# Kernel optimization log

Measured on AMD Instinct MI355X. Metric: run time of the kernel, lower is better.

## Reference

```python
import jax, jax.numpy as jnp
import numpy as np

BATCH, SEQ_L, H, N = 16, 2048, 512, 64
DT_MIN, DT_MAX = 1e-3, 1e-1


def setup_inputs() -> dict:
    key = jax.random.key(0)
    ks = jax.random.split(key, 6)
    u = jax.random.normal(ks[0], (BATCH, SEQ_L, H), dtype=jnp.float32)
    # S4D diagonal init: stable real part, linearly spaced imaginary frequencies
    Lambda_real = -0.5 * jnp.ones((N,), dtype=jnp.float32)
    Lambda_imag = jnp.pi * jnp.arange(N, dtype=jnp.float32)
    B_real = jax.random.normal(ks[1], (H, N), dtype=jnp.float32) * (N ** -0.5)
    B_imag = jnp.zeros((H, N), dtype=jnp.float32)
    C_real = jax.random.normal(ks[2], (H, N), dtype=jnp.float32) * 0.5
    C_imag = jax.random.normal(ks[3], (H, N), dtype=jnp.float32) * 0.5
    log_dt = (jax.random.uniform(ks[4], (H,), dtype=jnp.float32)
              * (np.float32(np.log(DT_MAX)) - np.float32(np.log(DT_MIN)))
              + np.float32(np.log(DT_MIN)))
    D = jax.random.normal(ks[5], (H,), dtype=jnp.float32) * 0.01
    return {"u": u, "Lambda_real": Lambda_real, "Lambda_imag": Lambda_imag,
            "B_real": B_real, "B_imag": B_imag, "C_real": C_real,
            "C_imag": C_imag, "log_dt": log_dt, "D": D}


def reference(u, Lambda_real, Lambda_imag, B_real, B_imag, C_real, C_imag, log_dt, D):
    # u: (B, L, H)
    Lseq = u.shape[1]
    Lam = Lambda_real + 1j * Lambda_imag            # (N,)
    Bc = B_real + 1j * B_imag                        # (H, N)
    Cc = C_real + 1j * C_imag                        # (H, N)
    dt = jnp.exp(log_dt)                             # (H,)

    # ZOH discretization (matches step(): Ab = exp(dt*Lam), Bb = B*(Ab-1)/(Lam+eps))
    dtA = dt[:, None] * Lam[None, :]                 # (H, N)
    Ab = jnp.exp(dtA)
    Bb = Bc * (Ab - 1.0) / (Lam[None, :] + 1e-8)

    # Vandermonde over all channels at once: V[h,n,l] = exp(dt_h * Lam_n * l)
    ell = jnp.arange(Lseq, dtype=jnp.float32)
    V = jnp.exp(dtA[:, :, None] * ell[None, None, :])  # (H, N, L) complex
    K = jnp.einsum('hn,hnl->hl', Cc * Bb, V).real       # (H, L) real kernel

    # Causal FFT convolution along time
    x = jnp.swapaxes(u, -1, -2)                      # (B, H, L)
    nfft = 2 * Lseq
    Xf = jnp.fft.rfft(x, n=nfft)                     # (B, H, nfft/2+1)
    Kf = jnp.fft.rfft(K, n=nfft)                     # (H, nfft/2+1)
    y = jnp.fft.irfft(Xf * Kf[None], n=nfft)[..., :Lseq]

    y = y + x * D[None, :, None]                     # skip connection
    return jnp.swapaxes(y, -1, -2)                   # (B, L, H)
```

## Files before the change

### kernel.cpp

```cpp
#include <hip/hip_runtime.h>
#include <hip/hip_bf16.h>


#define BSZ 16
#define LSEQ 2048
#define HCH 512
#define NST 64
#define NF 4096

__device__ __forceinline__ int WD(int i) { return 2 * i + ((i >> 4) << 1); }

__device__ __forceinline__ float2 cadd(float2 a, float2 b) { return make_float2(a.x + b.x, a.y + b.y); }
__device__ __forceinline__ float2 csub(float2 a, float2 b) { return make_float2(a.x - b.x, a.y - b.y); }
__device__ __forceinline__ float2 cmul(float2 a, float c, float s) {
    return make_float2(a.x * c - a.y * s, a.x * s + a.y * c);
}
__device__ __forceinline__ float2 cmul2(float2 a, float2 b) {
    return make_float2(a.x * b.x - a.y * b.y, a.x * b.y + a.y * b.x);
}

__device__ __forceinline__ void sincos_red(float a, float* s, float* c) {
    double ad = (double)a;
    double q = rint(ad * 0.15915494309189535);
    float r = (float)(ad - q * 6.283185307179586);
    __sincosf(r, s, c);
}

template <bool INV>
__device__ __forceinline__ void dft8_tail(float2 t0, float2 t1, float2 t2, float2 t3,
                                          float2 t4, float2 t5, float2 t6, float2 t7,
                                          float2& A0, float2& A1, float2& A2, float2& A3,
                                          float2& A4, float2& A5, float2& A6, float2& A7)
{
    const float S = 0.70710678118654752f;
    float2 u0 = cadd(t0, t2), u2 = csub(t0, t2);
    float2 u1 = cadd(t1, t3), u3 = csub(t1, t3);
    A0 = cadd(u0, u1); A4 = csub(u0, u1);
    if constexpr (!INV) {
        A2 = make_float2(u2.x + u3.y, u2.y - u3.x);
        A6 = make_float2(u2.x - u3.y, u2.y + u3.x);
    } else {
        A2 = make_float2(u2.x - u3.y, u2.y + u3.x);
        A6 = make_float2(u2.x + u3.y, u2.y - u3.x);
    }
    float2 b0 = t4, b1, b2, b3;
    if constexpr (!INV) {
        b1 = make_float2(S * (t5.x + t5.y), S * (t5.y - t5.x));
        b2 = make_float2(t6.y, -t6.x);
        b3 = make_float2(S * (t7.y - t7.x), -S * (t7.x + t7.y));
    } else {
        b1 = make_float2(S * (t5.x - t5.y), S * (t5.y + t5.x));
        b2 = make_float2(-t6.y, t6.x);
        b3 = make_float2(-S * (t7.x + t7.y), S * (t7.x - t7.y));
    }
    float2 v0 = cadd(b0, b2), v2 = csub(b0, b2);
    float2 v1 = cadd(b1, b3), v3 = csub(b1, b3);
    A1 = cadd(v0, v1); A5 = csub(v0, v1);
    if constexpr (!INV) {
        A3 = make_float2(v2.x + v3.y, v2.y - v3.x);
        A7 = make_float2(v2.x - v3.y, v2.y + v3.x);
    } else {
        A3 = make_float2(v2.x - v3.y, v2.y + v3.x);
        A7 = make_float2(v2.x + v3.y, v2.y - v3.x);
    }
}

template <int SIDX, bool INV, bool HALF, int NT>
__device__ __forceinline__ void fft8_stage(float* z, int t)
{
    constexpr int lgQ = 9 - 3 * SIDX;
    constexpr int Q = 1 << lgQ;
    constexpr int ITERS = 512 / NT;
    const float asc = -1.5339807878856412e-3f * (float)(1 << (3 * SIDX));
#pragma unroll
    for (int it = 0; it < ITERS; ++it) {
        const int bb = t + NT * it;
        const int j = bb & (Q - 1);
        const int base = ((bb >> lgQ) << (lgQ + 3)) + j;
        float s1, c1;
        __sincosf(asc * (float)j, &s1, &c1);
        if constexpr (INV) s1 = -s1;
        const float c2 = c1 * c1 - s1 * s1, s2 = 2.f * c1 * s1;
        const float c3 = c1 * c2 - s1 * s2, s3 = c1 * s2 + s1 * c2;
        const float c4 = c2 * c2 - s2 * s2, s4 = 2.f * c2 * s2;
        const float c5 = c2 * c3 - s2 * s3, s5 = c2 * s3 + s2 * c3;
        const float c6 = c3 * c3 - s3 * s3, s6 = 2.f * c3 * s3;
        const float c7 = c3 * c4 - s3 * s4, s7 = c3 * s4 + s3 * c4;
        float2 a0 = *(float2*)&z[WD(base + 0 * Q)];
        float2 a1 = *(float2*)&z[WD(base + 1 * Q)];
        float2 a2 = *(float2*)&z[WD(base + 2 * Q)];
        float2 a3 = *(float2*)&z[WD(base + 3 * Q)];
        float2 a4, a5, a6, a7;
        if constexpr (!(HALF && !INV)) {
            a4 = *(float2*)&z[WD(base + 4 * Q)];
            a5 = *(float2*)&z[WD(base + 5 * Q)];
            a6 = *(float2*)&z[WD(base + 6 * Q)];
            a7 = *(float2*)&z[WD(base + 7 * Q)];
        }
        if constexpr (INV) {
            a1 = cmul(a1, c1, s1); a2 = cmul(a2, c2, s2); a3 = cmul(a3, c3, s3);
            a4 = cmul(a4, c4, s4); a5 = cmul(a5, c5, s5); a6 = cmul(a6, c6, s6);
            a7 = cmul(a7, c7, s7);
        }
        float2 t0, t1, t2, t3, t4, t5, t6, t7;
        if constexpr (HALF && !INV) {
            t0 = a0; t4 = a0; t1 = a1; t5 = a1; t2 = a2; t6 = a2; t3 = a3; t7 = a3;
        } else {
            t0 = cadd(a0, a4); t4 = csub(a0, a4);
            t1 = cadd(a1, a5); t5 = csub(a1, a5);
            t2 = cadd(a2, a6); t6 = csub(a2, a6);
            t3 = cadd(a3, a7); t7 = csub(a3, a7);
        }
        float2 A0, A1, A2, A3, A4, A5, A6, A7;
        dft8_tail<INV>(t0, t1, t2, t3, t4, t5, t6, t7, A0, A1, A2, A3, A4, A5, A6, A7);
        if constexpr (!INV) {
            A1 = cmul(A1, c1, s1); A2 = cmul(A2, c2, s2); A3 = cmul(A3, c3, s3);
            A4 = cmul(A4, c4, s4); A5 = cmul(A5, c5, s5); A6 = cmul(A6, c6, s6);
            A7 = cmul(A7, c7, s7);
        }
        *(float2*)&z[WD(base + 0 * Q)] = A0;
        *(float2*)&z[WD(base + 1 * Q)] = A1;
        *(float2*)&z[WD(base + 2 * Q)] = A2;
        *(float2*)&z[WD(base + 3 * Q)] = A3;
        if constexpr (!(HALF && INV)) {
            *(float2*)&z[WD(base + 4 * Q)] = A4;
            *(float2*)&z[WD(base + 5 * Q)] = A5;
            *(float2*)&z[WD(base + 6 * Q)] = A6;
            *(float2*)&z[WD(base + 7 * Q)] = A7;
        }
    }
}

template <int NT>
__device__ __forceinline__ void mid_stage(float* z, const float2* __restrict__ kf, int t)
{
    constexpr int ITERS = 512 / NT;
#pragma unroll
    for (int it = 0; it < ITERS; ++it) {
        const int bb = t + NT * it;
        const int base = bb * 8;
        float2 a[8];
#pragma unroll
        for (int r = 0; r < 8; ++r) a[r] = *(float2*)&z[WD(base + r)];
        float2 t0 = cadd(a[0], a[4]), t4 = csub(a[0], a[4]);
        float2 t1 = cadd(a[1], a[5]), t5 = csub(a[1], a[5]);
        float2 t2 = cadd(a[2], a[6]), t6 = csub(a[2], a[6]);
        float2 t3 = cadd(a[3], a[7]), t7 = csub(a[3], a[7]);
        float2 A0, A1, A2, A3, A4, A5, A6, A7;
        dft8_tail<false>(t0, t1, t2, t3, t4, t5, t6, t7, A0, A1, A2, A3, A4, A5, A6, A7);
        const float2* kp = kf + base;
        A0 = cmul2(A0, kp[0]); A1 = cmul2(A1, kp[1]);
        A2 = cmul2(A2, kp[2]); A3 = cmul2(A3, kp[3]);
        A4 = cmul2(A4, kp[4]); A5 = cmul2(A5, kp[5]);
        A6 = cmul2(A6, kp[6]); A7 = cmul2(A7, kp[7]);
        t0 = cadd(A0, A4); t4 = csub(A0, A4);
        t1 = cadd(A1, A5); t5 = csub(A1, A5);
        t2 = cadd(A2, A6); t6 = csub(A2, A6);
        t3 = cadd(A3, A7); t7 = csub(A3, A7);
        float2 X0, X1, X2, X3, X4, X5, X6, X7;
        dft8_tail<true>(t0, t1, t2, t3, t4, t5, t6, t7, X0, X1, X2, X3, X4, X5, X6, X7);
        *(float2*)&z[WD(base + 0)] = X0;
        *(float2*)&z[WD(base + 1)] = X1;
        *(float2*)&z[WD(base + 2)] = X2;
        *(float2*)&z[WD(base + 3)] = X3;
        *(float2*)&z[WD(base + 4)] = X4;
        *(float2*)&z[WD(base + 5)] = X5;
        *(float2*)&z[WD(base + 6)] = X6;
        *(float2*)&z[WD(base + 7)] = X7;
    }
}

__global__ __launch_bounds__(512) void k_front(const float* __restrict__ lam_r,
                                               const float* __restrict__ lam_i,
                                               const float* __restrict__ Br,
                                               const float* __restrict__ Bi,
                                               const float* __restrict__ Cr,
                                               const float* __restrict__ Ci,
                                               const float* __restrict__ log_dt,
                                               float* __restrict__ gKf,
                                               const float* __restrict__ u,
                                               float* __restrict__ gut)
{
    const int bid = blockIdx.x;
    const int t = threadIdx.x;
    __shared__ float lds[8704];
    __shared__ float sWr[NST], sWi[NST], sAr[NST], sAi[NST], sDr[NST], sDi[NST];

    if (bid < HCH) {
        const int h = bid;
        if (t < NST) {
            const int n = t;
            float lr = lam_r[n], li = lam_i[n];
            float dt = __expf(log_dt[h]);
            float dar = dt * lr;
            float dai = dt * li;
            float e = __expf(dar);
            float sn, cs; sincos_red(dai, &sn, &cs);
            float Ar = e * cs, Ai = e * sn;
            float nr = Ar - 1.0f, ni = Ai;
            float br = Br[h * NST + n], bi = Bi[h * NST + n];
            float tr = br * nr - bi * ni;
            float ti = br * ni + bi * nr;
            float dr = lr + 1e-8f, di = li;
            float den = dr * dr + di * di;
            float bbr = (tr * dr + ti * di) / den;
            float bbi = (ti * dr - tr * di) / den;
            float cr = Cr[h * NST + n], ci = Ci[h * NST + n];
            sWr[n] = cr * bbr - ci * bbi;
            sWi[n] = cr * bbi + ci * bbr;
            sAr[n] = Ar; sAi[n] = Ai;
            sDr[n] = dar; sDi[n] = dai;
        }
        __syncthreads();

        const int l0 = 4 * t;
        float acc[4] = {0.f, 0.f, 0.f, 0.f};
        const float fl0 = (float)l0;
        for (int n = 0; n < NST; ++n) {
            float dar = sDr[n], dai = sDi[n];
            float ang = dai * fl0;
            float sn, cs; sincos_red(ang, &sn, &cs);
            float e = __expf(dar * fl0);
            float pr = e * cs, pi = e * sn;
            float Ar = sAr[n], Ai = sAi[n];
            float wr = sWr[n], wi = sWi[n];
#pragma unroll
            for (int k = 0; k < 4; ++k) {
                acc[k] += wr * pr - wi * pi;
                float npr = pr * Ar - pi * Ai;
                pi = pr * Ai + pi * Ar;
                pr = npr;
            }
        }
        *(float2*)&lds[WD(l0 + 0)] = make_float2(acc[0], 0.f);
        *(float2*)&lds[WD(l0 + 1)] = make_float2(acc[1], 0.f);
        *(float2*)&lds[WD(l0 + 2)] = make_float2(acc[2], 0.f);
        *(float2*)&lds[WD(l0 + 3)] = make_float2(acc[3], 0.f);
        __syncthreads();

        fft8_stage<0, false, true , 512>(lds, t); __syncthreads();
        fft8_stage<1, false, false, 512>(lds, t); __syncthreads();
        fft8_stage<2, false, false, 512>(lds, t); __syncthreads();
        fft8_stage<3, false, false, 512>(lds, t); __syncthreads();

        float2* outp = (float2*)gKf + (size_t)h * NF;
#pragma unroll
        for (int i = 0; i < 8; ++i) {
            int idx = t + 512 * i;
            outp[idx] = *(float2*)&lds[WD(idx)];
        }
    } else {
        float (*tile)[65] = (float (*)[65])lds;
        const int tid2 = bid - HCH;
        const int b  = tid2 >> 8;
        const int ht = ((tid2 >> 5) & 7) * 64;
        const int lt = (tid2 & 31) * 64;
        const int tx = t & 15;
        const int ty = t >> 4;
        const float* inb = u + (size_t)b * LSEQ * HCH;
        float* outb = gut + (size_t)b * HCH * LSEQ;
#pragma unroll
        for (int i = 0; i < 2; ++i) {
            int r = ty + 32 * i;
            float4 v = *(const float4*)&inb[(size_t)(lt + r) * HCH + ht + 4 * tx];
            tile[r][4 * tx + 0] = v.x;
            tile[r][4 * tx + 1] = v.y;
            tile[r][4 * tx + 2] = v.z;
            tile[r][4 * tx + 3] = v.w;
        }
        __syncthreads();
#pragma unroll
        for (int i = 0; i < 2; ++i) {
            int rp = ty + 32 * i;
            float4 o = make_float4(tile[4 * tx + 0][rp], tile[4 * tx + 1][rp],
                                   tile[4 * tx + 2][rp], tile[4 * tx + 3][rp]);
            *(float4*)&outb[(size_t)(ht + rp) * LSEQ + lt + 4 * tx] = o;
        }
    }
}

__global__ __launch_bounds__(256) void k_transpose_bwd(const float* __restrict__ in,
                                                       float* __restrict__ out)
{
    __shared__ float tile[64][65];
    const int b  = blockIdx.z;
    const int lt = blockIdx.x * 64;
    const int ht = blockIdx.y * 64;
    const int tx = threadIdx.x;
    const int ty = threadIdx.y;
    const float* inb = in + (size_t)b * HCH * LSEQ;
    float* outb = out + (size_t)b * LSEQ * HCH;
#pragma unroll
    for (int i = 0; i < 4; ++i) {
        int r = ty + 16 * i;
        float4 v = *(const float4*)&inb[(size_t)(ht + r) * LSEQ + lt + 4 * tx];
        tile[r][4 * tx + 0] = v.x;
        tile[r][4 * tx + 1] = v.y;
        tile[r][4 * tx + 2] = v.z;
        tile[r][4 * tx + 3] = v.w;
    }
    __syncthreads();
#pragma unroll
    for (int i = 0; i < 4; ++i) {
        int rp = ty + 16 * i;
        float4 o = make_float4(tile[4 * tx + 0][rp], tile[4 * tx + 1][rp],
                               tile[4 * tx + 2][rp], tile[4 * tx + 3][rp]);
        *(float4*)&outb[(size_t)(lt + rp) * HCH + ht + 4 * tx] = o;
    }
}

__global__ __launch_bounds__(512, 4) void k_fftconv(float* __restrict__ gut,
                                                    const float* __restrict__ gKf,
                                                    const float* __restrict__ gD)
{
    const int bid = blockIdx.x;
    const int b = bid >> 9;
    const int h = bid & (HCH - 1);
    const int t = threadIdx.x;
    __shared__ float z[8704];

    float* row0 = gut + ((size_t)(b * HCH) + h) * LSEQ;
    float* row1 = gut + ((size_t)((b + 8) * HCH) + h) * LSEQ;

    float4 u0k = ((const float4*)row0)[t];
    float4 u1k = ((const float4*)row1)[t];
    {
        int l = 4 * t;
        *(float2*)&z[WD(l + 0)] = make_float2(u0k.x, u1k.x);
        *(float2*)&z[WD(l + 1)] = make_float2(u0k.y, u1k.y);
        *(float2*)&z[WD(l + 2)] = make_float2(u0k.z, u1k.z);
        *(float2*)&z[WD(l + 3)] = make_float2(u0k.w, u1k.w);
    }
    __syncthreads();

    fft8_stage<0, false, true , 512>(z, t); __syncthreads();
    fft8_stage<1, false, false, 512>(z, t); __syncthreads();
    fft8_stage<2, false, false, 512>(z, t); __syncthreads();
    mid_stage<512>(z, (const float2*)gKf + (size_t)h * NF, t); __syncthreads();
    fft8_stage<2, true, false, 512>(z, t); __syncthreads();
    fft8_stage<1, true, false, 512>(z, t); __syncthreads();
    fft8_stage<0, true, true , 512>(z, t); __syncthreads();

    const float sc = 1.0f / 4096.0f;
    const float Dh = gD[h];
    {
        int l = 4 * t;
        float2 z0 = *(float2*)&z[WD(l + 0)];
        float2 z1 = *(float2*)&z[WD(l + 1)];
        float2 z2 = *(float2*)&z[WD(l + 2)];
        float2 z3 = *(float2*)&z[WD(l + 3)];
        float4 o0 = make_float4(z0.x * sc + Dh * u0k.x, z1.x * sc + Dh * u0k.y,
                                z2.x * sc + Dh * u0k.z, z3.x * sc + Dh * u0k.w);
        float4 o1 = make_float4(z0.y * sc + Dh * u1k.x, z1.y * sc + Dh * u1k.y,
                                z2.y * sc + Dh * u1k.z, z3.y * sc + Dh * u1k.w);
        ((float4*)row0)[t] = o0;
        ((float4*)row1)[t] = o1;
    }
}

extern "C" void kernel_launch(void* const* d_in, const int* in_sizes, int n_in,
                              void* d_out, int out_size, void* d_ws, size_t ws_size,
                              hipStream_t stream)
{
    const float* u      = (const float*)d_in[0];
    const float* lam_r  = (const float*)d_in[1];
    const float* lam_i  = (const float*)d_in[2];
    const float* Br     = (const float*)d_in[3];
    const float* Bi     = (const float*)d_in[4];
    const float* Cr     = (const float*)d_in[5];
    const float* Ci     = (const float*)d_in[6];
    const float* log_dt = (const float*)d_in[7];
    const float* Dv     = (const float*)d_in[8];

    float* gut = (float*)d_ws;
    float* gKf = (float*)d_out;

    k_front<<<HCH + 4096, 512, 0, stream>>>(lam_r, lam_i, Br, Bi, Cr, Ci, log_dt,
                                            gKf, u, gut);
    k_fftconv<<<BSZ / 2 * HCH, 512, 0, stream>>>(gut, gKf, Dv);
    k_transpose_bwd<<<dim3(LSEQ / 64, HCH / 64, BSZ), dim3(16, 16, 1), 0, stream>>>(gut, (float*)d_out);
}
```

Measured before the change: 221.2 us.

## Process two packed FFT pairs per block, sharing twiddles and kernel spectrum

The FFT convolution kernel now handles four batch rows per block (two complex-packed FFTs) instead of two. The per-thread twiddle factors and the Kf spectrum loads are reused across both FFTs, and the grid shrinks to 2048 blocks. Shared memory switches from a padded layout to an XOR-swizzled float2 layout, which removes the padding. LDS use roughly doubles per block (64KB), which can cut occupancy, and the launch-bounds hint of 4 blocks may no longer be achievable.

```diff
diff --git a/kernel.cpp b/kernel.cpp
--- a/kernel.cpp
+++ b/kernel.cpp
@@ -9,6 +9,7 @@
 #define NF 4096
 
 __device__ __forceinline__ int WD(int i) { return 2 * i + ((i >> 4) << 1); }
+__device__ __forceinline__ int CWS(int i) { return i ^ (((i >> 4) & 7) << 1); }
 
 __device__ __forceinline__ float2 cadd(float2 a, float2 b) { return make_float2(a.x + b.x, a.y + b.y); }
 __device__ __forceinline__ float2 csub(float2 a, float2 b) { return make_float2(a.x - b.x, a.y - b.y); }
@@ -131,24 +132,94 @@
     }
 }
 
-template <int NT>
-__device__ __forceinline__ void mid_stage(float* z, const float2* __restrict__ kf, int t)
-{
-    constexpr int ITERS = 512 / NT;
-#pragma unroll
-    for (int it = 0; it < ITERS; ++it) {
-        const int bb = t + NT * it;
-        const int base = bb * 8;
+template <int SIDX, bool INV, bool HALF>
+__device__ __forceinline__ void fft8_stage2(float2* __restrict__ za,
+                                            float2* __restrict__ zb, int t)
+{
+    constexpr int lgQ = 9 - 3 * SIDX;
+    constexpr int Q = 1 << lgQ;
+    const float asc = -1.5339807878856412e-3f * (float)(1 << (3 * SIDX));
+    const int j = t & (Q - 1);
+    const int base = ((t >> lgQ) << (lgQ + 3)) + j;
+    float s1, c1;
+    __sincosf(asc * (float)j, &s1, &c1);
+    if constexpr (INV) s1 = -s1;
+    const float c2 = c1 * c1 - s1 * s1, s2 = 2.f * c1 * s1;
+    const float c3 = c1 * c2 - s1 * s2, s3 = c1 * s2 + s1 * c2;
+    const float c4 = c2 * c2 - s2 * s2, s4 = 2.f * c2 * s2;
+    const float c5 = c2 * c3 - s2 * s3, s5 = c2 * s3 + s2 * c3;
+    const float c6 = c3 * c3 - s3 * s3, s6 = 2.f * c3 * s3;
+    const float c7 = c3 * c4 - s3 * s4, s7 = c3 * s4 + s3 * c4;
+    float2* const zs[2] = {za, zb};
+#pragma unroll
+    for (int rr = 0; rr < 2; ++rr) {
+        float2* __restrict__ z = zs[rr];
+        float2 a0 = z[CWS(base + 0 * Q)];
+        float2 a1 = z[CWS(base + 1 * Q)];
+        float2 a2 = z[CWS(base + 2 * Q)];
+        float2 a3 = z[CWS(base + 3 * Q)];
+        float2 a4, a5, a6, a7;
+        if constexpr (!(HALF && !INV)) {
+            a4 = z[CWS(base + 4 * Q)];
+            a5 = z[CWS(base + 5 * Q)];
+            a6 = z[CWS(base + 6 * Q)];
+            a7 = z[CWS(base + 7 * Q)];
+        }
+        if constexpr (INV) {
+            a1 = cmul(a1, c1, s1); a2 = cmul(a2, c2, s2); a3 = cmul(a3, c3, s3);
+            a4 = cmul(a4, c4, s4); a5 = cmul(a5, c5, s5); a6 = cmul(a6, c6, s6);
+            a7 = cmul(a7, c7, s7);
+        }
+        float2 t0, t1, t2, t3, t4, t5, t6, t7;
+        if constexpr (HALF && !INV) {
+            t0 = a0; t4 = a0; t1 = a1; t5 = a1; t2 = a2; t6 = a2; t3 = a3; t7 = a3;
+        } else {
+            t0 = cadd(a0, a4); t4 = csub(a0, a4);
+            t1 = cadd(a1, a5); t5 = csub(a1, a5);
+            t2 = cadd(a2, a6); t6 = csub(a2, a6);
+            t3 = cadd(a3, a7); t7 = csub(a3, a7);
+        }
+        float2 A0, A1, A2, A3, A4, A5, A6, A7;
+        dft8_tail<INV>(t0, t1, t2, t3, t4, t5, t6, t7, A0, A1, A2, A3, A4, A5, A6, A7);
+        if constexpr (!INV) {
+            A1 = cmul(A1, c1, s1); A2 = cmul(A2, c2, s2); A3 = cmul(A3, c3, s3);
+            A4 = cmul(A4, c4, s4); A5 = cmul(A5, c5, s5); A6 = cmul(A6, c6, s6);
+            A7 = cmul(A7, c7, s7);
+        }
+        z[CWS(base + 0 * Q)] = A0;
+        z[CWS(base + 1 * Q)] = A1;
+        z[CWS(base + 2 * Q)] = A2;
+        z[CWS(base + 3 * Q)] = A3;
+        if constexpr (!(HALF && INV)) {
+            z[CWS(base + 4 * Q)] = A4;
+            z[CWS(base + 5 * Q)] = A5;
+            z[CWS(base + 6 * Q)] = A6;
+            z[CWS(base + 7 * Q)] = A7;
+        }
+    }
+}
+
+__device__ __forceinline__ void mid_stage2(float2* __restrict__ z0,
+                                           float2* __restrict__ z1,
+                                           const float2* __restrict__ kf, int t)
+{
+    const int base = t * 8;
+    float2 kp[8];
+#pragma unroll
+    for (int r = 0; r < 8; ++r) kp[r] = kf[base + r];
+    float2* const zs[2] = {z0, z1};
+#pragma unroll
+    for (int rr = 0; rr < 2; ++rr) {
+        float2* __restrict__ z = zs[rr];
         float2 a[8];
 #pragma unroll
-        for (int r = 0; r < 8; ++r) a[r] = *(float2*)&z[WD(base + r)];
+        for (int r = 0; r < 8; ++r) a[r] = z[CWS(base + r)];
         float2 t0 = cadd(a[0], a[4]), t4 = csub(a[0], a[4]);
         float2 t1 = cadd(a[1], a[5]), t5 = csub(a[1], a[5]);
         float2 t2 = cadd(a[2], a[6]), t6 = csub(a[2], a[6]);
         float2 t3 = cadd(a[3], a[7]), t7 = csub(a[3], a[7]);
         float2 A0, A1, A2, A3, A4, A5, A6, A7;
         dft8_tail<false>(t0, t1, t2, t3, t4, t5, t6, t7, A0, A1, A2, A3, A4, A5, A6, A7);
-        const float2* kp = kf + base;
         A0 = cmul2(A0, kp[0]); A1 = cmul2(A1, kp[1]);
         A2 = cmul2(A2, kp[2]); A3 = cmul2(A3, kp[3]);
         A4 = cmul2(A4, kp[4]); A5 = cmul2(A5, kp[5]);
@@ -159,14 +230,14 @@
         t3 = cadd(A3, A7); t7 = csub(A3, A7);
         float2 X0, X1, X2, X3, X4, X5, X6, X7;
         dft8_tail<true>(t0, t1, t2, t3, t4, t5, t6, t7, X0, X1, X2, X3, X4, X5, X6, X7);
-        *(float2*)&z[WD(base + 0)] = X0;
-        *(float2*)&z[WD(base + 1)] = X1;
-        *(float2*)&z[WD(base + 2)] = X2;
-        *(float2*)&z[WD(base + 3)] = X3;
-        *(float2*)&z[WD(base + 4)] = X4;
-        *(float2*)&z[WD(base + 5)] = X5;
-        *(float2*)&z[WD(base + 6)] = X6;
-        *(float2*)&z[WD(base + 7)] = X7;
+        z[CWS(base + 0)] = X0;
+        z[CWS(base + 1)] = X1;
+        z[CWS(base + 2)] = X2;
+        z[CWS(base + 3)] = X3;
+        z[CWS(base + 4)] = X4;
+        z[CWS(base + 5)] = X5;
+        z[CWS(base + 6)] = X6;
+        z[CWS(base + 7)] = X7;
     }
 }
 
@@ -309,52 +380,64 @@
     }
 }
 
-__global__ __launch_bounds__(512, 4) void k_fftconv(float* __restrict__ gut,
-                                                    const float* __restrict__ gKf,
-                                                    const float* __restrict__ gD)
+__global__ __launch_bounds__(512, 4) void k_conv2(float* __restrict__ gut,
+                                                  const float* __restrict__ gKf,
+                                                  const float* __restrict__ gD)
 {
     const int bid = blockIdx.x;
-    const int b = bid >> 9;
-    const int h = bid & (HCH - 1);
+    const int bp = bid & 3;
+    const int h  = bid >> 2;
     const int t = threadIdx.x;
-    __shared__ float z[8704];
-
-    float* row0 = gut + ((size_t)(b * HCH) + h) * LSEQ;
-    float* row1 = gut + ((size_t)((b + 8) * HCH) + h) * LSEQ;
-
-    float4 u0k = ((const float4*)row0)[t];
-    float4 u1k = ((const float4*)row1)[t];
+    __shared__ float2 zz0[4096];
+    __shared__ float2 zz1[4096];
+
+    float* rA0 = gut + ((size_t)(bp       * HCH) + h) * LSEQ;
+    float* rA1 = gut + ((size_t)((bp + 8) * HCH) + h) * LSEQ;
+    float* rB0 = gut + ((size_t)((bp + 4) * HCH) + h) * LSEQ;
+    float* rB1 = gut + ((size_t)((bp + 12)* HCH) + h) * LSEQ;
+
+    float4 uA0 = ((const float4*)rA0)[t];
+    float4 uA1 = ((const float4*)rA1)[t];
+    float4 uB0 = ((const float4*)rB0)[t];
+    float4 uB1 = ((const float4*)rB1)[t];
     {
         int l = 4 * t;
-        *(float2*)&z[WD(l + 0)] = make_float2(u0k.x, u1k.x);
-        *(float2*)&z[WD(l + 1)] = make_float2(u0k.y, u1k.y);
-        *(float2*)&z[WD(l + 2)] = make_float2(u0k.z, u1k.z);
-        *(float2*)&z[WD(l + 3)] = make_float2(u0k.w, u1k.w);
+        zz0[CWS(l + 0)] = make_float2(uA0.x, uA1.x);
+        zz0[CWS(l + 1)] = make_float2(uA0.y, uA1.y);
+        zz0[CWS(l + 2)] = make_float2(uA0.z, uA1.z);
+        zz0[CWS(l + 3)] = make_float2(uA0.w, uA1.w);
+        zz1[CWS(l + 0)] = make_float2(uB0.x, uB1.x);
+        zz1[CWS(l + 1)] = make_float2(uB0.y, uB1.y);
+        zz1[CWS(l + 2)] = make_float2(uB0.z, uB1.z);
+        zz1[CWS(l + 3)] = make_float2(uB0.w, uB1.w);
     }
     __syncthreads();
 
-    fft8_stage<0, false, true , 512>(z, t); __syncthreads();
-    fft8_stage<1, false, false, 512>(z, t); __syncthreads();
-    fft8_stage<2, false, false, 512>(z, t); __syncthreads();
-    mid_stage<512>(z, (const float2*)gKf + (size_t)h * NF, t); __syncthreads();
-    fft8_stage<2, true, false, 512>(z, t); __syncthreads();
-    fft8_stage<1, true, false, 512>(z, t); __syncthreads();
-    fft8_stage<0, true, true , 512>(z, t); __syncthreads();
+    const float2* kfh = (const float2*)gKf + (size_t)h * NF;
+    fft8_stage2<0, false, true >(zz0, zz1, t); __syncthreads();
+    fft8_stage2<1, false, false>(zz0, zz1, t); __syncthreads();
+    fft8_stage2<2, false, false>(zz0, zz1, t); __syncthreads();
+    mid_stage2(zz0, zz1, kfh, t); __syncthreads();
+    fft8_stage2<2, true, false>(zz0, zz1, t); __syncthreads();
+    fft8_stage2<1, true, false>(zz0, zz1, t); __syncthreads();
+    fft8_stage2<0, true, true >(zz0, zz1, t); __syncthreads();
 
     const float sc = 1.0f / 4096.0f;
     const float Dh = gD[h];
     {
         int l = 4 * t;
-        float2 z0 = *(float2*)&z[WD(l + 0)];
-        float2 z1 = *(float2*)&z[WD(l + 1)];
-        float2 z2 = *(float2*)&z[WD(l + 2)];
-        float2 z3 = *(float2*)&z[WD(l + 3)];
-        float4 o0 = make_float4(z0.x * sc + Dh * u0k.x, z1.x * sc + Dh * u0k.y,
-                                z2.x * sc + Dh * u0k.z, z3.x * sc + Dh * u0k.w);
-        float4 o1 = make_float4(z0.y * sc + Dh * u1k.x, z1.y * sc + Dh * u1k.y,
-                                z2.y * sc + Dh * u1k.z, z3.y * sc + Dh * u1k.w);
-        ((float4*)row0)[t] = o0;
-        ((float4*)row1)[t] = o1;
+        float2 a0 = zz0[CWS(l + 0)], a1 = zz0[CWS(l + 1)];
+        float2 a2 = zz0[CWS(l + 2)], a3 = zz0[CWS(l + 3)];
+        float2 b0 = zz1[CWS(l + 0)], b1 = zz1[CWS(l + 1)];
+        float2 b2 = zz1[CWS(l + 2)], b3 = zz1[CWS(l + 3)];
+        ((float4*)rA0)[t] = make_float4(a0.x * sc + Dh * uA0.x, a1.x * sc + Dh * uA0.y,
+                                        a2.x * sc + Dh * uA0.z, a3.x * sc + Dh * uA0.w);
+        ((float4*)rA1)[t] = make_float4(a0.y * sc + Dh * uA1.x, a1.y * sc + Dh * uA1.y,
+                                        a2.y * sc + Dh * uA1.z, a3.y * sc + Dh * uA1.w);
+        ((float4*)rB0)[t] = make_float4(b0.x * sc + Dh * uB0.x, b1.x * sc + Dh * uB0.y,
+                                        b2.x * sc + Dh * uB0.z, b3.x * sc + Dh * uB0.w);
+        ((float4*)rB1)[t] = make_float4(b0.y * sc + Dh * uB1.x, b1.y * sc + Dh * uB1.y,
+                                        b2.y * sc + Dh * uB1.z, b3.y * sc + Dh * uB1.w);
     }
 }
 
@@ -377,6 +460,6 @@
 
     k_front<<<HCH + 4096, 512, 0, stream>>>(lam_r, lam_i, Br, Bi, Cr, Ci, log_dt,
                                             gKf, u, gut);
-    k_fftconv<<<BSZ / 2 * HCH, 512, 0, stream>>>(gut, gKf, Dv);
+    k_conv2<<<4 * HCH, 512, 0, stream>>>(gut, gKf, Dv);
     k_transpose_bwd<<<dim3(LSEQ / 64, HCH / 64, BSZ), dim3(16, 16, 1), 0, stream>>>(gut, (float*)d_out);
 }
```

Result: slower. 241.7 us (+9.2%).

## Fold skip term into kernel spectrum and finish inverse FFT in registers

Applied to the files above, without the earlier changes.

The D skip connection is folded into the kernel's frequency response by adding D to the real part of every Kf bin, so k_fftconv no longer keeps the input values in registers for the epilogue. The last forward stage in k_front writes straight from registers, and the last inverse stage in k_fftconv computes only the four needed outputs in registers, dropping an LDS round trip and a barrier. Launch bounds for k_fftconv are raised to ask for more resident blocks. The tail stores become scalar strided writes rather than float4, which may cost some store efficiency.

```diff
diff --git a/kernel.cpp b/kernel.cpp
--- a/kernel.cpp
+++ b/kernel.cpp
@@ -170,6 +170,41 @@
     }
 }
 
+__device__ __forceinline__ void fft8_stage0_inv_reg(const float* z, int t,
+                                                    float2& A0, float2& A1,
+                                                    float2& A2, float2& A3)
+{
+    const float asc = -1.5339807878856412e-3f;
+    const int j = t;
+    const int base = t;
+    float s1, c1;
+    __sincosf(asc * (float)j, &s1, &c1);
+    s1 = -s1;
+    const float c2 = c1 * c1 - s1 * s1, s2 = 2.f * c1 * s1;
+    const float c3 = c1 * c2 - s1 * s2, s3 = c1 * s2 + s1 * c2;
+    const float c4 = c2 * c2 - s2 * s2, s4 = 2.f * c2 * s2;
+    const float c5 = c2 * c3 - s2 * s3, s5 = c2 * s3 + s2 * c3;
+    const float c6 = c3 * c3 - s3 * s3, s6 = 2.f * c3 * s3;
+    const float c7 = c3 * c4 - s3 * s4, s7 = c3 * s4 + s3 * c4;
+    float2 a0 = *(const float2*)&z[WD(base + 0 * 512)];
+    float2 a1 = *(const float2*)&z[WD(base + 1 * 512)];
+    float2 a2 = *(const float2*)&z[WD(base + 2 * 512)];
+    float2 a3 = *(const float2*)&z[WD(base + 3 * 512)];
+    float2 a4 = *(const float2*)&z[WD(base + 4 * 512)];
+    float2 a5 = *(const float2*)&z[WD(base + 5 * 512)];
+    float2 a6 = *(const float2*)&z[WD(base + 6 * 512)];
+    float2 a7 = *(const float2*)&z[WD(base + 7 * 512)];
+    a1 = cmul(a1, c1, s1); a2 = cmul(a2, c2, s2); a3 = cmul(a3, c3, s3);
+    a4 = cmul(a4, c4, s4); a5 = cmul(a5, c5, s5); a6 = cmul(a6, c6, s6);
+    a7 = cmul(a7, c7, s7);
+    float2 t0 = cadd(a0, a4), t4 = csub(a0, a4);
+    float2 t1 = cadd(a1, a5), t5 = csub(a1, a5);
+    float2 t2 = cadd(a2, a6), t6 = csub(a2, a6);
+    float2 t3 = cadd(a3, a7), t7 = csub(a3, a7);
+    float2 A4d, A5d, A6d, A7d;
+    dft8_tail<true>(t0, t1, t2, t3, t4, t5, t6, t7, A0, A1, A2, A3, A4d, A5d, A6d, A7d);
+}
+
 __global__ __launch_bounds__(512) void k_front(const float* __restrict__ lam_r,
                                                const float* __restrict__ lam_i,
                                                const float* __restrict__ Br,
@@ -177,6 +212,7 @@
                                                const float* __restrict__ Cr,
                                                const float* __restrict__ Ci,
                                                const float* __restrict__ log_dt,
+                                               const float* __restrict__ gD,
                                                float* __restrict__ gKf,
                                                const float* __restrict__ u,
                                                float* __restrict__ gut)
@@ -241,13 +277,29 @@
         fft8_stage<0, false, true , 512>(lds, t); __syncthreads();
         fft8_stage<1, false, false, 512>(lds, t); __syncthreads();
         fft8_stage<2, false, false, 512>(lds, t); __syncthreads();
-        fft8_stage<3, false, false, 512>(lds, t); __syncthreads();
-
-        float2* outp = (float2*)gKf + (size_t)h * NF;
-#pragma unroll
-        for (int i = 0; i < 8; ++i) {
-            int idx = t + 512 * i;
-            outp[idx] = *(float2*)&lds[WD(idx)];
+
+        {
+            const float Dh = gD[h];
+            const int base = 8 * t;
+            float2 a0 = *(float2*)&lds[WD(base + 0)];
+            float2 a1 = *(float2*)&lds[WD(base + 1)];
+            float2 a2 = *(float2*)&lds[WD(base + 2)];
+            float2 a3 = *(float2*)&lds[WD(base + 3)];
+            float2 a4 = *(float2*)&lds[WD(base + 4)];
+            float2 a5 = *(float2*)&lds[WD(base + 5)];
+            float2 a6 = *(float2*)&lds[WD(base + 6)];
+            float2 a7 = *(float2*)&lds[WD(base + 7)];
+            float2 t0 = cadd(a0, a4), t4 = csub(a0, a4);
+            float2 t1 = cadd(a1, a5), t5 = csub(a1, a5);
+            float2 t2 = cadd(a2, a6), t6 = csub(a2, a6);
+            float2 t3 = cadd(a3, a7), t7 = csub(a3, a7);
+            float2 A0, A1, A2, A3, A4, A5, A6, A7;
+            dft8_tail<false>(t0, t1, t2, t3, t4, t5, t6, t7, A0, A1, A2, A3, A4, A5, A6, A7);
+            float4* o4 = (float4*)((float2*)gKf + (size_t)h * NF + base);
+            o4[0] = make_float4(A0.x + Dh, A0.y, A1.x + Dh, A1.y);
+            o4[1] = make_float4(A2.x + Dh, A2.y, A3.x + Dh, A3.y);
+            o4[2] = make_float4(A4.x + Dh, A4.y, A5.x + Dh, A5.y);
+            o4[3] = make_float4(A6.x + Dh, A6.y, A7.x + Dh, A7.y);
         }
     } else {
         float (*tile)[65] = (float (*)[65])lds;
@@ -309,9 +361,8 @@
     }
 }
 
-__global__ __launch_bounds__(512, 4) void k_fftconv(float* __restrict__ gut,
-                                                    const float* __restrict__ gKf,
-                                                    const float* __restrict__ gD)
+__global__ __launch_bounds__(512, 8) void k_fftconv(float* __restrict__ gut,
+                                                    const float* __restrict__ gKf)
 {
     const int bid = blockIdx.x;
     const int b = bid >> 9;
@@ -322,9 +373,9 @@
     float* row0 = gut + ((size_t)(b * HCH) + h) * LSEQ;
     float* row1 = gut + ((size_t)((b + 8) * HCH) + h) * LSEQ;
 
-    float4 u0k = ((const float4*)row0)[t];
-    float4 u1k = ((const float4*)row1)[t];
     {
+        float4 u0k = ((const float4*)row0)[t];
+        float4 u1k = ((const float4*)row1)[t];
         int l = 4 * t;
         *(float2*)&z[WD(l + 0)] = make_float2(u0k.x, u1k.x);
         *(float2*)&z[WD(l + 1)] = make_float2(u0k.y, u1k.y);
@@ -339,23 +390,15 @@
     mid_stage<512>(z, (const float2*)gKf + (size_t)h * NF, t); __syncthreads();
     fft8_stage<2, true, false, 512>(z, t); __syncthreads();
     fft8_stage<1, true, false, 512>(z, t); __syncthreads();
-    fft8_stage<0, true, true , 512>(z, t); __syncthreads();
+
+    float2 A0, A1, A2, A3;
+    fft8_stage0_inv_reg(z, t, A0, A1, A2, A3);
 
     const float sc = 1.0f / 4096.0f;
-    const float Dh = gD[h];
-    {
-        int l = 4 * t;
-        float2 z0 = *(float2*)&z[WD(l + 0)];
-        float2 z1 = *(float2*)&z[WD(l + 1)];
-        float2 z2 = *(float2*)&z[WD(l + 2)];
-        float2 z3 = *(float2*)&z[WD(l + 3)];
-        float4 o0 = make_float4(z0.x * sc + Dh * u0k.x, z1.x * sc + Dh * u0k.y,
-                                z2.x * sc + Dh * u0k.z, z3.x * sc + Dh * u0k.w);
-        float4 o1 = make_float4(z0.y * sc + Dh * u1k.x, z1.y * sc + Dh * u1k.y,
-                                z2.y * sc + Dh * u1k.z, z3.y * sc + Dh * u1k.w);
-        ((float4*)row0)[t] = o0;
-        ((float4*)row1)[t] = o1;
-    }
+    row0[t +    0] = A0.x * sc;  row1[t +    0] = A0.y * sc;
+    row0[t +  512] = A1.x * sc;  row1[t +  512] = A1.y * sc;
+    row0[t + 1024] = A2.x * sc;  row1[t + 1024] = A2.y * sc;
+    row0[t + 1536] = A3.x * sc;  row1[t + 1536] = A3.y * sc;
 }
 
 extern "C" void kernel_launch(void* const* d_in, const int* in_sizes, int n_in,
@@ -376,7 +419,7 @@
     float* gKf = (float*)d_out;
 
     k_front<<<HCH + 4096, 512, 0, stream>>>(lam_r, lam_i, Br, Bi, Cr, Ci, log_dt,
-                                            gKf, u, gut);
-    k_fftconv<<<BSZ / 2 * HCH, 512, 0, stream>>>(gut, gKf, Dv);
+                                            Dv, gKf, u, gut);
+    k_fftconv<<<BSZ / 2 * HCH, 512, 0, stream>>>(gut, gKf);
     k_transpose_bwd<<<dim3(LSEQ / 64, HCH / 64, BSZ), dim3(16, 16, 1), 0, stream>>>(gut, (float*)d_out);
 }
```

Result: slower. 277.1 us (+25.3%).
